# Performance work log

Measured on AMD Instinct MI355X. Metric: run time of the kernel, lower is better.

## Reference

```python
import jax, jax.numpy as jnp
import numpy as np

TOP_K = 8

def setup_inputs() -> dict:
    key = jax.random.key(0)
    k1, k2 = jax.random.split(key)
    hidden_states = jax.random.normal(k1, (4, 4096, 2048), dtype=jnp.float32)
    weight = jax.random.normal(k2, (64, 2048), dtype=jnp.float32) * 0.02
    return {"hidden_states": hidden_states, "weight": weight}

def reference(hidden_states, weight):
    b, s, h = hidden_states.shape
    x = hidden_states.reshape(-1, h).astype(jnp.float32)   # [T, H]
    logits = jnp.einsum('th,eh->te', x, weight.astype(jnp.float32))  # [T, E]
    scores = jax.nn.softmax(logits, axis=-1)               # greedy router: softmax then top-k
    topk_weights, topk_idx = jax.lax.top_k(scores, TOP_K)  # [T, k]
    # renormalize top-k probabilities (norm_topk_prob)
    topk_weights = topk_weights / jnp.sum(topk_weights, axis=-1, keepdims=True)
    return topk_weights, topk_idx
```

## Files before the change

kernel.cpp:

```cpp
#include <hip/hip_runtime.h>
#include <math.h>


#define H_DIM 2048
#define N_EXP 64
#define TOPK 8

typedef __attribute__((ext_vector_type(8))) short bf16x8;
typedef __attribute__((ext_vector_type(4))) float f32x4;

union FragU { uint4 q; unsigned u[4]; bf16x8 s; };

__device__ inline unsigned cvt_pk_bf16(float lo, float hi) {
  unsigned d;
  asm("v_cvt_pk_bf16_f32 %0, %1, %2" : "=v"(d) : "v"(lo), "v"(hi));
  return d;
}

__device__ inline void split3(const float* e, unsigned* dh, unsigned* dm,
                              unsigned* dl) {
#pragma unroll
  for (int p = 0; p < 4; ++p) {
    const float f0 = e[2 * p], f1 = e[2 * p + 1];
    const unsigned h = cvt_pk_bf16(f0, f1);
    const float r0 = f0 - __uint_as_float(h << 16);
    const float r1 = f1 - __uint_as_float(h & 0xffff0000u);
    const unsigned m = cvt_pk_bf16(r0, r1);
    const float s0 = r0 - __uint_as_float(m << 16);
    const float s1 = r1 - __uint_as_float(m & 0xffff0000u);
    dl[p] = cvt_pk_bf16(s0, s1);
    dh[p] = h;
    dm[p] = m;
  }
}

__global__ __launch_bounds__(256) void w_split_kernel(
    const float* __restrict__ w, uint4* __restrict__ ws) {
  const int id = blockIdx.x * 256 + threadIdx.x;
  const int l = id & 63;
  const int nt = (id >> 6) & 3;
  const int ksg = id >> 8;
  const int n = nt * 16 + (l & 15);
  const int kb = ksg * 32 + ((l >> 4) << 3);
  const float* wr = w + (size_t)n * H_DIM + kb;
  const float4 a = *(const float4*)(wr);
  const float4 b = *(const float4*)(wr + 4);
  const float e[8] = {a.x, a.y, a.z, a.w, b.x, b.y, b.z, b.w};
  unsigned dh[4], dm[4], dl[4];
  split3(e, dh, dm, dl);
  const int base = (ksg * 12 + nt * 3) * 64 + l;
  ws[base] = make_uint4(dh[0], dh[1], dh[2], dh[3]);
  ws[base + 64] = make_uint4(dm[0], dm[1], dm[2], dm[3]);
  ws[base + 128] = make_uint4(dl[0], dl[1], dl[2], dl[3]);
}

__global__ __launch_bounds__(512, 2) void moe_gate_kernel(
    const float* __restrict__ x, const uint4* __restrict__ wf_g,
    float* __restrict__ out, int n_tokens) {
  __shared__ float part[8 * 2048];
  __shared__ float logits[N_EXP * 64];

  const int tid = threadIdx.x;
  const int l = tid & 63;
  const int w = tid >> 6;
  const int tp = w & 1;
  const int kq = w >> 1;
  const int t0 = blockIdx.x * 64;

  const float* xp0 =
      x + (size_t)(t0 + tp * 32 + (l & 15)) * H_DIM + kq * 512 + ((l >> 4) << 3);
  const float* xp1 = xp0 + (size_t)16 * H_DIM;

  f32x4 acc[2][4];
#pragma unroll
  for (int t = 0; t < 2; ++t)
#pragma unroll
    for (int nt = 0; nt < 4; ++nt) acc[t][nt] = (f32x4){0.f, 0.f, 0.f, 0.f};

  float4 xa[2][2], xb[2][2], xc[2][2];
  xa[0][0] = *(const float4*)(xp0);
  xa[0][1] = *(const float4*)(xp0 + 4);
  xa[1][0] = *(const float4*)(xp1);
  xa[1][1] = *(const float4*)(xp1 + 4);
  xb[0][0] = *(const float4*)(xp0 + 32);
  xb[0][1] = *(const float4*)(xp0 + 36);
  xb[1][0] = *(const float4*)(xp1 + 32);
  xb[1][1] = *(const float4*)(xp1 + 36);

  const uint4* wbase = wf_g + (size_t)(kq * 16) * 768 + l;

#pragma unroll 1
  for (int s = 0; s < 16; ++s) {
    uint4 wf[12];
    const uint4* wb = wbase + (size_t)s * 768;
#pragma unroll
    for (int i = 0; i < 12; ++i) wf[i] = wb[i * 64];

    if (s + 2 < 16) {
      const float* p0 = xp0 + (s + 2) * 32;
      const float* p1 = xp1 + (s + 2) * 32;
      xc[0][0] = *(const float4*)(p0);
      xc[0][1] = *(const float4*)(p0 + 4);
      xc[1][0] = *(const float4*)(p1);
      xc[1][1] = *(const float4*)(p1 + 4);
    }

    bf16x8 ah[2], am[2], al[2];
#pragma unroll
    for (int t = 0; t < 2; ++t) {
      const float4 v0 = xa[t][0], v1 = xa[t][1];
      const float e[8] = {v0.x, v0.y, v0.z, v0.w, v1.x, v1.y, v1.z, v1.w};
      FragU uh, um, ul;
      split3(e, uh.u, um.u, ul.u);
      ah[t] = uh.s;
      am[t] = um.s;
      al[t] = ul.s;
    }

#pragma unroll
    for (int nt = 0; nt < 4; ++nt) {
      FragU bh, bm, bl;
      bh.q = wf[nt * 3 + 0];
      bm.q = wf[nt * 3 + 1];
      bl.q = wf[nt * 3 + 2];
#pragma unroll
      for (int t = 0; t < 2; ++t) {
        f32x4 c = acc[t][nt];
        c = __builtin_amdgcn_mfma_f32_16x16x32_bf16(ah[t], bh.s, c, 0, 0, 0);
        c = __builtin_amdgcn_mfma_f32_16x16x32_bf16(am[t], bh.s, c, 0, 0, 0);
        c = __builtin_amdgcn_mfma_f32_16x16x32_bf16(ah[t], bm.s, c, 0, 0, 0);
        c = __builtin_amdgcn_mfma_f32_16x16x32_bf16(al[t], bh.s, c, 0, 0, 0);
        c = __builtin_amdgcn_mfma_f32_16x16x32_bf16(ah[t], bl.s, c, 0, 0, 0);
        c = __builtin_amdgcn_mfma_f32_16x16x32_bf16(am[t], bm.s, c, 0, 0, 0);
        acc[t][nt] = c;
      }
    }

#pragma unroll
    for (int t = 0; t < 2; ++t)
#pragma unroll
      for (int h = 0; h < 2; ++h) {
        xa[t][h] = xb[t][h];
        xb[t][h] = xc[t][h];
      }
  }

#pragma unroll
  for (int t = 0; t < 2; ++t)
#pragma unroll
    for (int nt = 0; nt < 4; ++nt)
      *(float4*)&part[w * 2048 + (t * 4 + nt) * 256 + l * 4] =
          make_float4(acc[t][nt][0], acc[t][nt][1], acc[t][nt][2],
                      acc[t][nt][3]);
  __syncthreads();

  for (int z = tid; z < N_EXP * 64; z += 512) {
    const int e = z >> 6, t64 = z & 63;
    const int tpz = t64 >> 5, tz = (t64 >> 4) & 1;
    const int qz = (t64 >> 2) & 3, rz = t64 & 3;
    const int lz = qz * 16 + (e & 15);
    const int ntz = e >> 4;
    const int idx = (tz * 4 + ntz) * 256 + lz * 4 + rz;
    float v = ((part[(0 * 2 + tpz) * 2048 + idx] +
                part[(1 * 2 + tpz) * 2048 + idx]) +
               (part[(2 * 2 + tpz) * 2048 + idx] +
                part[(3 * 2 + tpz) * 2048 + idx]));
    logits[z] = v;
  }
  __syncthreads();

  if (w != 0) return;

  float lg[N_EXP];
#pragma unroll
  for (int e = 0; e < N_EXP; ++e) lg[e] = logits[e * 64 + l];

  float bw[TOPK];
  int bi[TOPK];
#pragma unroll
  for (int k = 0; k < TOPK; ++k) {
    float m = lg[0];
    int mi = 0;
#pragma unroll
    for (int e = 1; e < N_EXP; ++e) {
      if (lg[e] > m) {
        m = lg[e];
        mi = e;
      }
    }
    bw[k] = m;
    bi[k] = mi;
#pragma unroll
    for (int e = 0; e < N_EXP; ++e)
      if (e == mi) lg[e] = -INFINITY;
  }

  const float mx = bw[0];
  float ew[TOPK];
  float s = 0.f;
#pragma unroll
  for (int k = 0; k < TOPK; ++k) {
    ew[k] = expf(bw[k] - mx);
    s += ew[k];
  }
  const float inv = 1.f / s;

  float4 w0, w1, i0, i1;
  w0.x = ew[0] * inv; w0.y = ew[1] * inv; w0.z = ew[2] * inv; w0.w = ew[3] * inv;
  w1.x = ew[4] * inv; w1.y = ew[5] * inv; w1.z = ew[6] * inv; w1.w = ew[7] * inv;
  i0.x = (float)bi[0]; i0.y = (float)bi[1]; i0.z = (float)bi[2]; i0.w = (float)bi[3];
  i1.x = (float)bi[4]; i1.y = (float)bi[5]; i1.z = (float)bi[6]; i1.w = (float)bi[7];

  const int t = t0 + l;
  float4* ow = reinterpret_cast<float4*>(out + (size_t)t * TOPK);
  ow[0] = w0;
  ow[1] = w1;
  float4* oi =
      reinterpret_cast<float4*>(out + (size_t)n_tokens * TOPK + (size_t)t * TOPK);
  oi[0] = i0;
  oi[1] = i1;
}

extern "C" void kernel_launch(void* const* d_in, const int* in_sizes, int n_in,
                              void* d_out, int out_size, void* d_ws,
                              size_t ws_size, hipStream_t stream) {
  const float* x = (const float*)d_in[0];
  const float* w = (const float*)d_in[1];
  float* out = (float*)d_out;
  const int n_tokens = in_sizes[0] / H_DIM;
  w_split_kernel<<<64, 256, 0, stream>>>(w, (uint4*)d_ws);
  const int n_blocks = n_tokens / 64;
  moe_gate_kernel<<<n_blocks, 512, 0, stream>>>(x, (const uint4*)d_ws, out,
                                                n_tokens);
}
```

Baseline: 212.6 us.

## Halve tokens per block and split K across all eight waves

Each block now handles 32 tokens instead of 64. All eight waves split the hidden dimension eight ways rather than two token halves by four K-quarters, and the cross-wave reduction sums eight partials. Launch bounds request four blocks per CU and the grid doubles, aiming for more parallelism and latency hiding on the memory-bound x stream. In exchange, each weight fragment is reused across fewer tokens, so total weight-load traffic doubles, and the LDS footprint (about 72KB per block) may still cap occupancy below the requested four blocks.

```diff
diff --git a/kernel.cpp b/kernel.cpp
--- a/kernel.cpp
+++ b/kernel.cpp
@@ -5,6 +5,7 @@
 #define H_DIM 2048
 #define N_EXP 64
 #define TOPK 8
+#define TOK 32
 
 typedef __attribute__((ext_vector_type(8))) short bf16x8;
 typedef __attribute__((ext_vector_type(4))) float f32x4;
@@ -54,21 +55,20 @@
   ws[base + 128] = make_uint4(dl[0], dl[1], dl[2], dl[3]);
 }
 
-__global__ __launch_bounds__(512, 2) void moe_gate_kernel(
+__global__ __launch_bounds__(512, 4) void moe_gate_kernel(
     const float* __restrict__ x, const uint4* __restrict__ wf_g,
     float* __restrict__ out, int n_tokens) {
   __shared__ float part[8 * 2048];
-  __shared__ float logits[N_EXP * 64];
+  __shared__ float logits[N_EXP * TOK];
 
   const int tid = threadIdx.x;
   const int l = tid & 63;
   const int w = tid >> 6;
-  const int tp = w & 1;
-  const int kq = w >> 1;
-  const int t0 = blockIdx.x * 64;
+  const int kq = __builtin_amdgcn_readfirstlane(w);
+  const int t0 = blockIdx.x * TOK;
 
   const float* xp0 =
-      x + (size_t)(t0 + tp * 32 + (l & 15)) * H_DIM + kq * 512 + ((l >> 4) << 3);
+      x + (size_t)(t0 + (l & 15)) * H_DIM + kq * 256 + ((l >> 4) << 3);
   const float* xp1 = xp0 + (size_t)16 * H_DIM;
 
   f32x4 acc[2][4];
@@ -87,16 +87,16 @@
   xb[1][0] = *(const float4*)(xp1 + 32);
   xb[1][1] = *(const float4*)(xp1 + 36);
 
-  const uint4* wbase = wf_g + (size_t)(kq * 16) * 768 + l;
+  const uint4* wbase = wf_g + (size_t)(kq * 8) * 768 + l;
 
 #pragma unroll 1
-  for (int s = 0; s < 16; ++s) {
+  for (int s = 0; s < 8; ++s) {
     uint4 wf[12];
     const uint4* wb = wbase + (size_t)s * 768;
 #pragma unroll
     for (int i = 0; i < 12; ++i) wf[i] = wb[i * 64];
 
-    if (s + 2 < 16) {
+    if (s + 2 < 8) {
       const float* p0 = xp0 + (s + 2) * 32;
       const float* p1 = xp1 + (s + 2) * 32;
       xc[0][0] = *(const float4*)(p0);
@@ -154,26 +154,24 @@
                       acc[t][nt][3]);
   __syncthreads();
 
-  for (int z = tid; z < N_EXP * 64; z += 512) {
-    const int e = z >> 6, t64 = z & 63;
-    const int tpz = t64 >> 5, tz = (t64 >> 4) & 1;
-    const int qz = (t64 >> 2) & 3, rz = t64 & 3;
-    const int lz = qz * 16 + (e & 15);
-    const int ntz = e >> 4;
-    const int idx = (tz * 4 + ntz) * 256 + lz * 4 + rz;
-    float v = ((part[(0 * 2 + tpz) * 2048 + idx] +
-                part[(1 * 2 + tpz) * 2048 + idx]) +
-               (part[(2 * 2 + tpz) * 2048 + idx] +
-                part[(3 * 2 + tpz) * 2048 + idx]));
+  for (int z = tid; z < N_EXP * TOK; z += 512) {
+    const int e = z >> 5, t32 = z & 31;
+    const int tz = t32 >> 4, r16 = t32 & 15;
+    const int q = r16 >> 2, rz = r16 & 3;
+    const int idx = (tz * 4 + (e >> 4)) * 256 + (q * 16 + (e & 15)) * 4 + rz;
+    float v = ((part[0 * 2048 + idx] + part[1 * 2048 + idx]) +
+               (part[2 * 2048 + idx] + part[3 * 2048 + idx])) +
+              ((part[4 * 2048 + idx] + part[5 * 2048 + idx]) +
+               (part[6 * 2048 + idx] + part[7 * 2048 + idx]));
     logits[z] = v;
   }
   __syncthreads();
 
-  if (w != 0) return;
+  if (tid >= TOK) return;
 
   float lg[N_EXP];
 #pragma unroll
-  for (int e = 0; e < N_EXP; ++e) lg[e] = logits[e * 64 + l];
+  for (int e = 0; e < N_EXP; ++e) lg[e] = logits[e * TOK + tid];
 
   float bw[TOPK];
   int bi[TOPK];
@@ -211,7 +209,7 @@
   i0.x = (float)bi[0]; i0.y = (float)bi[1]; i0.z = (float)bi[2]; i0.w = (float)bi[3];
   i1.x = (float)bi[4]; i1.y = (float)bi[5]; i1.z = (float)bi[6]; i1.w = (float)bi[7];
 
-  const int t = t0 + l;
+  const int t = t0 + tid;
   float4* ow = reinterpret_cast<float4*>(out + (size_t)t * TOPK);
   ow[0] = w0;
   ow[1] = w1;
@@ -229,7 +227,7 @@
   float* out = (float*)d_out;
   const int n_tokens = in_sizes[0] / H_DIM;
   w_split_kernel<<<64, 256, 0, stream>>>(w, (uint4*)d_ws);
-  const int n_blocks = n_tokens / 64;
+  const int n_blocks = n_tokens / TOK;
   moe_gate_kernel<<<n_blocks, 512, 0, stream>>>(x, (const uint4*)d_ws, out,
                                                 n_tokens);
 }
```

Measured after the change: 261.9 us. 1.23x slower.
